# Kernel tuning notes

Measured on AMD Instinct MI355X. Metric: run time of the kernel, lower is better.

Reference implementation:

```python
import jax, jax.numpy as jnp
import numpy as np

N_HEADS = 8
DIM_HEAD = 64
SCALE = DIM_HEAD ** -0.5


def setup_inputs() -> dict:
    key = jax.random.key(0)
    ks = jax.random.split(key, 7)
    B, C, H, W = 2, 512, 64, 64
    inner = N_HEADS * DIM_HEAD  # 512
    x = jax.random.normal(ks[0], (B, C, H, W), dtype=jnp.float32)
    context = jax.random.normal(ks[1], (B, C, H, W), dtype=jnp.float32)
    # kaiming_normal fan_out for 1x1 conv: std = sqrt(2 / out_channels)
    std_qkv = (2.0 / inner) ** 0.5
    std_o = (2.0 / C) ** 0.5
    Wq = jax.random.normal(ks[2], (inner, C), dtype=jnp.float32) * std_qkv
    Wk = jax.random.normal(ks[3], (inner, C), dtype=jnp.float32) * std_qkv
    Wv = jax.random.normal(ks[4], (inner, C), dtype=jnp.float32) * std_qkv
    Wo = jax.random.normal(ks[5], (C, inner), dtype=jnp.float32) * std_o
    return {
        'x': x, 'context': context,
        'Wq': Wq, 'bq': jnp.zeros((inner,), jnp.float32),
        'Wk': Wk, 'bk': jnp.zeros((inner,), jnp.float32),
        'Wv': Wv, 'bv': jnp.zeros((inner,), jnp.float32),
        'Wo': Wo, 'bo': jnp.zeros((C,), jnp.float32),
    }


def _attention(x, context, Wq, bq, Wk, bk, Wv, bv, Wo, bo):
    b, c, h, w = x.shape
    s = h * w
    # 1x1 conv == per-pixel channel matmul. Flatten spatial: [b, s, c]
    xf = x.reshape(b, c, s).transpose(0, 2, 1)
    cf = context.reshape(b, c, s).transpose(0, 2, 1)
    q = jnp.einsum('bsc,ec->bse', xf, Wq) + bq  # [b, s, inner]
    k = jnp.einsum('bsc,ec->bse', cf, Wk) + bk
    v = jnp.einsum('bsc,ec->bse', cf, Wv) + bv
    # split heads: [b, n, s, d]
    def split(t):
        return t.reshape(b, s, N_HEADS, DIM_HEAD).transpose(0, 2, 1, 3)
    q, k, v = split(q), split(k), split(v)
    sim = jnp.einsum('bnid,bnjd->bnij', q, k) * SCALE  # [b, n, s, s]
    attn = jax.nn.softmax(sim, axis=-1)
    out = jnp.einsum('bnij,bnjd->bnid', attn, v)  # [b, n, s, d]
    # merge heads back to channels: 'b n s d -> b (n d) s'
    out = out.transpose(0, 2, 1, 3).reshape(b, s, N_HEADS * DIM_HEAD)
    out = jnp.einsum('bse,ce->bsc', out, Wo) + bo  # output proj (1x1 conv)
    return out.transpose(0, 2, 1).reshape(b, c, h, w)


def reference(x, context, Wq, bq, Wk, bk, Wv, bv, Wo, bo):
    return _attention(x, context, Wq, bq, Wk, bk, Wv, bv, Wo, bo)
```

## Files before the change

### kernel.cpp

```cpp
#include <hip/hip_runtime.h>
#include <cstdint>


typedef __bf16 bf16x8 __attribute__((ext_vector_type(8)));
typedef __bf16 bf16x4 __attribute__((ext_vector_type(4)));
typedef float f32x4 __attribute__((ext_vector_type(4)));
typedef unsigned short u16x8 __attribute__((ext_vector_type(8)));
typedef unsigned short u16x4 __attribute__((ext_vector_type(4)));

#define AS1 __attribute__((address_space(1)))
#define AS3 __attribute__((address_space(3)))

__device__ __forceinline__ void async16(const void* g, void* l) {
  __builtin_amdgcn_global_load_lds((const AS1 void*)g, (AS3 void*)l, 16, 0, 0);
}

__device__ __forceinline__ uint16_t f2bf(float f) {
  union { float f; uint32_t u; } a;
  a.f = f;
  uint32_t r = a.u + 0x7fffu + ((a.u >> 16) & 1u);
  return (uint16_t)(r >> 16);
}

__device__ __forceinline__ float bf2f(uint16_t u) {
  union { uint32_t u; float f; } a;
  a.u = (uint32_t)u << 16;
  return a.f;
}

__global__ __launch_bounds__(256) void cvt_w(
    const float* __restrict__ W0, const float* __restrict__ W1,
    const float* __restrict__ W2, const float* __restrict__ W3,
    uint16_t* __restrict__ O0, uint16_t* __restrict__ O1,
    uint16_t* __restrict__ O2, uint16_t* __restrict__ O3) {
  const float* W[4] = {W0, W1, W2, W3};
  uint16_t* O[4] = {O0, O1, O2, O3};
  const int w = blockIdx.y;
  const int i = (blockIdx.x * 256 + threadIdx.x) * 4;
  float4 v = *(const float4*)&W[w][i];
  u16x4 o = {f2bf(v.x), f2bf(v.y), f2bf(v.z), f2bf(v.w)};
  *(u16x4*)&O[w][i] = o;
}

__global__ __launch_bounds__(256) void transpose_cs(
    const float* __restrict__ x, const float* __restrict__ ctx,
    uint16_t* __restrict__ xT, uint16_t* __restrict__ cT) {
  const int zz = blockIdx.z;
  const float* src = (zz < 2 ? x : ctx) + (size_t)(zz & 1) * 512 * 4096;
  uint16_t* dst = (zz < 2 ? xT : cT) + (size_t)(zz & 1) * 4096 * 512;
  const int s0 = blockIdx.x * 64, c0 = blockIdx.y * 64;
  __shared__ uint16_t tile[64][80];
  const int t = threadIdx.x;
  for (int p = 0; p < 2; ++p) {
    int u = p * 256 + t;
    int r = u >> 3, cg = (u & 7) * 8;
    const float* sp = &src[(size_t)(c0 + r) * 4096 + s0 + cg];
    float4 v0 = *(const float4*)sp;
    float4 v1 = *(const float4*)(sp + 4);
    u16x8 o = {f2bf(v0.x), f2bf(v0.y), f2bf(v0.z), f2bf(v0.w),
               f2bf(v1.x), f2bf(v1.y), f2bf(v1.z), f2bf(v1.w)};
    *(u16x8*)&tile[r][cg] = o;
  }
  __syncthreads();
  for (int p = 0; p < 2; ++p) {
    int u = p * 256 + t;
    int sr = u >> 3, cg = (u & 7) * 8;
    u16x8 v;
    for (int j = 0; j < 8; ++j) v[j] = tile[cg + j][sr];
    *(u16x8*)&dst[(size_t)(s0 + sr) * 512 + c0 + cg] = v;
  }
}

struct QkvArgs {
  const uint16_t* A[3]; long long sA[3];
  const uint16_t* B[3]; long long sB[3];
  uint16_t* C[3];       long long sC[3];
  const float* bias[3];
  float os[3];
  long long ldC[3]; int lx[3]; int brow[3];
};

__global__ __launch_bounds__(256) void gemm_qkv(QkvArgs ga) {
  constexpr int K = 512;
  __shared__ uint16_t At[128 * 32];
  __shared__ uint16_t Bt[128 * 32];
  const int t = threadIdx.x, lane = t & 63, wave = t >> 6;
  const int lr = lane & 15, lq = lane >> 4;
  const int wm = (wave >> 1) * 64, wn = (wave & 1) * 64;
  const int sel = blockIdx.z >> 1, bat = blockIdx.z & 1;
  const int lx = ga.lx[sel], brow = ga.brow[sel];
  const long long ldC = ga.ldC[sel];
  const float os = ga.os[sel];
  const int n0 = (blockIdx.x & ((1 << lx) - 1)) * 128;
  const int m0 = (blockIdx.x >> lx) * 128;
  const uint16_t* A = ga.A[sel] + (size_t)bat * ga.sA[sel];
  const uint16_t* B = ga.B[sel] + (size_t)bat * ga.sB[sel];
  const float* bias = ga.bias[sel];
  f32x4 acc[4][4] = {};
  for (int k0 = 0; k0 < K; k0 += 32) {
    __syncthreads();
    for (int p = 0; p < 2; ++p) {
      int u = p * 256 + t;
      int r = u >> 2, c = (u & 3) * 8;
      async16(&A[(size_t)(m0 + r) * K + k0 + c], &At[p * 2048 + wave * 512]);
      async16(&B[(size_t)(n0 + r) * K + k0 + c], &Bt[p * 2048 + wave * 512]);
    }
    __builtin_amdgcn_s_waitcnt(0);
    __syncthreads();
    bf16x8 af[4], bfr[4];
    for (int i = 0; i < 4; ++i)
      af[i] = *(const bf16x8*)&At[(wm + i * 16 + lr) * 32 + lq * 8];
    for (int j = 0; j < 4; ++j)
      bfr[j] = *(const bf16x8*)&Bt[(wn + j * 16 + lr) * 32 + lq * 8];
    for (int i = 0; i < 4; ++i)
      for (int j = 0; j < 4; ++j)
        acc[i][j] = __builtin_amdgcn_mfma_f32_16x16x32_bf16(af[i], bfr[j], acc[i][j], 0, 0, 0);
  }
  uint16_t* C = ga.C[sel] + (size_t)bat * ga.sC[sel];
  for (int i = 0; i < 4; ++i)
    for (int j = 0; j < 4; ++j) {
      int row = m0 + wm + i * 16 + lq * 4;
      int col = n0 + wn + j * 16 + lr;
      float bc = brow ? 0.f : bias[col];
      u16x4 o;
      for (int r = 0; r < 4; ++r) {
        float val = (acc[i][j][r] + (brow ? bias[row + r] : bc)) * os;
        o[r] = f2bf(val);
      }
      *(u16x4*)&C[(size_t)col * ldC + row] = o;
    }
}

__global__ __launch_bounds__(256) void gemm_out(
    const uint16_t* __restrict__ Ob, long long sA,
    const uint16_t* __restrict__ Wo, float* __restrict__ Y, long long sC,
    const float* __restrict__ bias) {
  constexpr int K = 512;
  __shared__ uint16_t At[128 * 32];
  __shared__ uint16_t Bt[64 * 32];
  const int t = threadIdx.x, lane = t & 63, wave = t >> 6;
  const int lr = lane & 15, lq = lane >> 4;
  const int wm = (wave & 1) * 64, wn = (wave >> 1) * 32;
  const int m0 = blockIdx.y * 128, n0 = blockIdx.x * 64;
  const uint16_t* A = Ob + (size_t)blockIdx.z * sA;
  f32x4 acc[4][2] = {};
  for (int k0 = 0; k0 < K; k0 += 32) {
    __syncthreads();
    for (int p = 0; p < 2; ++p) {
      int u = p * 256 + t;
      int r = u >> 2, c = (u & 3) * 8;
      async16(&A[(size_t)(m0 + r) * K + k0 + c], &At[p * 2048 + wave * 512]);
    }
    {
      int r = t >> 2, c = (t & 3) * 8;
      async16(&Wo[(size_t)(n0 + r) * K + k0 + c], &Bt[wave * 512]);
    }
    __builtin_amdgcn_s_waitcnt(0);
    __syncthreads();
    bf16x8 af[4], bfr[2];
    for (int i = 0; i < 4; ++i)
      af[i] = *(const bf16x8*)&At[(wm + i * 16 + lr) * 32 + lq * 8];
    for (int j = 0; j < 2; ++j)
      bfr[j] = *(const bf16x8*)&Bt[(wn + j * 16 + lr) * 32 + lq * 8];
    for (int i = 0; i < 4; ++i)
      for (int j = 0; j < 2; ++j)
        acc[i][j] = __builtin_amdgcn_mfma_f32_16x16x32_bf16(af[i], bfr[j], acc[i][j], 0, 0, 0);
  }
  float* Cf = Y + (size_t)blockIdx.z * sC;
  for (int i = 0; i < 4; ++i)
    for (int j = 0; j < 2; ++j) {
      int row = m0 + wm + i * 16 + lq * 4;
      int col = n0 + wn + j * 16 + lr;
      float bb = bias[col];
      float4 o = {acc[i][j][0] + bb, acc[i][j][1] + bb,
                  acc[i][j][2] + bb, acc[i][j][3] + bb};
      *(float4*)&Cf[(size_t)col * 4096 + row] = o;
    }
}

__global__ __launch_bounds__(512, 4) void attn128(
    const uint16_t* __restrict__ Q, const uint16_t* __restrict__ K,
    const uint16_t* __restrict__ Vt, uint16_t* __restrict__ Ap,
    float* __restrict__ Lp) {
  constexpr int S = 4096, E = 512;
  const int b = blockIdx.z & 1, jh = blockIdx.z >> 1;
  const int h = blockIdx.y;
  const int i0 = blockIdx.x * 256;
  const int t = threadIdx.x, lane = t & 63, wave = t >> 6;
  const int lr = lane & 15, lq = lane >> 4;
  const size_t qkB = (size_t)b * S * E;
  const size_t vB = (size_t)b * E * S;
  __shared__ uint16_t Kl[2][64 * 64];
  __shared__ uint16_t Vl[2][64 * 64];

  const int qbase = i0 + wave * 32;
  bf16x8 qf[2][2];
  for (int g = 0; g < 2; ++g) {
    const size_t qo = qkB + (size_t)(qbase + g * 16 + lr) * E + h * 64 + lq * 8;
    qf[g][0] = *(const bf16x8*)&Q[qo];
    qf[g][1] = *(const bf16x8*)&Q[qo + 32];
  }
  f32x4 lsum[2] = {};
  f32x4 accOT[2][4] = {};
  const f32x4 fz = {0.f, 0.f, 0.f, 0.f};
  const int swz = (lr & 7);
  const int srr = t >> 3, ssc = ((t & 7) ^ (srr & 7)) * 8;

  const int jbeg = jh * (S / 2), jend = jbeg + S / 2;
  async16(&K[qkB + (size_t)(jbeg + srr) * E + h * 64 + ssc], &Kl[0][wave * 512]);
  async16(&Vt[vB + (size_t)(h * 64 + srr) * S + jbeg + ssc], &Vl[0][wave * 512]);
  __builtin_amdgcn_s_waitcnt(0);
  __syncthreads();

  int cur = 0;
  for (int j0 = jbeg; j0 < jend; j0 += 64) {
    if (j0 + 64 < jend) {
      async16(&K[qkB + (size_t)(j0 + 64 + srr) * E + h * 64 + ssc], &Kl[cur ^ 1][wave * 512]);
      async16(&Vt[vB + (size_t)(h * 64 + srr) * S + j0 + 64 + ssc], &Vl[cur ^ 1][wave * 512]);
    }
    const uint16_t* Kc = Kl[cur];
    const uint16_t* Vc = Vl[cur];
    f32x4 svt[2][4];
#pragma unroll
    for (int jn = 0; jn < 4; ++jn) {
      const int row = jn * 16 + lr;
      const int c0 = (lq ^ swz) * 8;
      bf16x8 ka0 = *(const bf16x8*)&Kc[row * 64 + c0];
      bf16x8 ka1 = *(const bf16x8*)&Kc[row * 64 + (c0 ^ 32)];
#pragma unroll
      for (int g = 0; g < 2; ++g) {
        f32x4 z = __builtin_amdgcn_mfma_f32_16x16x32_bf16(ka0, qf[g][0], fz, 0, 0, 0);
        z = __builtin_amdgcn_mfma_f32_16x16x32_bf16(ka1, qf[g][1], z, 0, 0, 0);
        svt[g][jn] = z;
      }
    }
    bf16x8 pa[2][2];
#pragma unroll
    for (int g = 0; g < 2; ++g) {
      uint32_t pk[4][2];
#pragma unroll
      for (int jn = 0; jn < 4; ++jn) {
        f32x4 p;
#pragma unroll
        for (int r = 0; r < 4; ++r) p[r] = __builtin_amdgcn_exp2f(svt[g][jn][r]);
        lsum[g] += p;
        asm("v_cvt_pk_bf16_f32 %0, %1, %2" : "=v"(pk[jn][0]) : "v"(p[0]), "v"(p[1]));
        asm("v_cvt_pk_bf16_f32 %0, %1, %2" : "=v"(pk[jn][1]) : "v"(p[2]), "v"(p[3]));
      }
#pragma unroll
      for (int half = 0; half < 2; ++half) {
        union { uint32_t w[4]; bf16x8 v; } f;
#pragma unroll
        for (int p_ = 0; p_ < 2; ++p_) {
          uint32_t a = pk[2 * half][p_];
          uint32_t c = pk[2 * half + 1][p_];
          asm("v_permlane32_swap_b32 %0, %1" : "+v"(a), "+v"(c));
          asm("v_permlane16_swap_b32 %0, %1" : "+v"(a), "+v"(c));
          f.w[p_] = a;
          f.w[2 + p_] = c;
        }
        pa[g][half] = f.v;
      }
    }
#pragma unroll
    for (int dn = 0; dn < 4; ++dn) {
      const int row = dn * 16 + lr;
      const int c0 = (lq ^ swz) * 8;
      bf16x8 v0 = *(const bf16x8*)&Vc[row * 64 + c0];
      bf16x8 v1 = *(const bf16x8*)&Vc[row * 64 + (c0 ^ 32)];
#pragma unroll
      for (int g = 0; g < 2; ++g) {
        accOT[g][dn] = __builtin_amdgcn_mfma_f32_16x16x32_bf16(v0, pa[g][0], accOT[g][dn], 0, 0, 0);
        accOT[g][dn] = __builtin_amdgcn_mfma_f32_16x16x32_bf16(v1, pa[g][1], accOT[g][dn], 0, 0, 0);
      }
    }
    __builtin_amdgcn_s_waitcnt(0);
    __syncthreads();
    cur ^= 1;
  }
  uint16_t* Aph = Ap + (size_t)jh * 2 * S * E;
  float* Lph = Lp + ((size_t)(jh * 2 + b) * 8 + h) * S;
  for (int g = 0; g < 2; ++g) {
    float lt = (lsum[g][0] + lsum[g][1]) + (lsum[g][2] + lsum[g][3]);
    lt += __shfl_xor(lt, 16);
    lt += __shfl_xor(lt, 32);
    if (lane < 16) Lph[qbase + g * 16 + lr] = lt;
    const size_t row = qbase + g * 16 + lr;
    for (int dn = 0; dn < 4; ++dn) {
      u16x4 o;
      for (int r = 0; r < 4; ++r) o[r] = f2bf(accOT[g][dn][r]);
      *(u16x4*)&Aph[qkB + row * E + h * 64 + dn * 16 + lq * 4] = o;
    }
  }
}

__global__ __launch_bounds__(256) void attn_combine(
    const uint16_t* __restrict__ Ap, const float* __restrict__ Lp,
    uint16_t* __restrict__ Ob) {
  constexpr int S = 4096, E = 512;
  const size_t HALF = (size_t)2 * S * E;
  const size_t idx = ((size_t)blockIdx.x * 256 + threadIdx.x) * 4;
  const int b = (int)(idx / ((size_t)S * E));
  const size_t rem = idx % ((size_t)S * E);
  const int s = (int)(rem / E), e = (int)(rem % E);
  const int h = e >> 6;
  const float l0 = Lp[((size_t)(0 * 2 + b) * 8 + h) * S + s];
  const float l1 = Lp[((size_t)(1 * 2 + b) * 8 + h) * S + s];
  const float inv = 1.f / (l0 + l1);
  u16x4 a0 = *(const u16x4*)&Ap[idx];
  u16x4 a1 = *(const u16x4*)&Ap[HALF + idx];
  u16x4 o;
  for (int r = 0; r < 4; ++r) o[r] = f2bf((bf2f(a0[r]) + bf2f(a1[r])) * inv);
  *(u16x4*)&Ob[idx] = o;
}

extern "C" void kernel_launch(void* const* d_in, const int* in_sizes, int n_in,
                              void* d_out, int out_size, void* d_ws, size_t ws_size,
                              hipStream_t stream) {
  const float* x   = (const float*)d_in[0];
  const float* ctx = (const float*)d_in[1];
  const float* Wq  = (const float*)d_in[2];
  const float* bq  = (const float*)d_in[3];
  const float* Wk  = (const float*)d_in[4];
  const float* bk  = (const float*)d_in[5];
  const float* Wv  = (const float*)d_in[6];
  const float* bv  = (const float*)d_in[7];
  const float* Wo  = (const float*)d_in[8];
  const float* bo  = (const float*)d_in[9];
  float* out = (float*)d_out;

  const size_t SZ = (size_t)2 * 4096 * 512;
  uint16_t* xT = (uint16_t*)d_ws;
  uint16_t* cT = xT + SZ;
  uint16_t* Qb = cT + SZ;
  uint16_t* Kb = Qb + SZ;
  uint16_t* Vb = Kb + SZ;
  uint16_t* Ob = Vb + SZ;
  uint16_t* Wqb = Ob + SZ;
  uint16_t* Wkb = Wqb + 512 * 512;
  uint16_t* Wvb = Wkb + 512 * 512;
  uint16_t* Wob = Wvb + 512 * 512;
  uint16_t* Ap  = Wob + 512 * 512;
  float*    Lp  = (float*)(Ap + 2 * SZ);
  const long long sIn = 4096LL * 512LL;
  const float slh = 0.125f * 1.44269504088896f;

  cvt_w<<<dim3(256, 4), 256, 0, stream>>>(Wq, Wk, Wv, Wo, Wqb, Wkb, Wvb, Wob);
  transpose_cs<<<dim3(64, 8, 4), 256, 0, stream>>>(x, ctx, xT, cT);
  QkvArgs qkv = {
      {Wqb, Wkb, cT}, {0, 0, sIn},
      {xT, cT, Wvb}, {sIn, sIn, 0},
      {Qb, Kb, Vb}, {sIn, sIn, sIn},
      {bq, bk, bv},
      {slh, 1.f, 1.f},
      {512, 512, 4096},
      {5, 5, 2},
      {1, 1, 0}};
  gemm_qkv<<<dim3(128, 1, 6), 256, 0, stream>>>(qkv);
  attn128<<<dim3(16, 8, 4), 512, 0, stream>>>(Qb, Kb, Vb, Ap, Lp);
  attn_combine<<<dim3(4096), 256, 0, stream>>>(Ap, Lp, Ob);
  gemm_out<<<dim3(8, 32, 2), 256, 0, stream>>>(Ob, sIn, Wob, out, sIn, bo);
}
```

Baseline: 224.8 us.

## Split attention keys into four chunks and compute row sums with MFMA

The attention kernel now splits the key range into quarters instead of halves, doubling the grid to 1024 blocks, and raises the launch-bounds occupancy hint. Row sums of the exponentials are accumulated with an MFMA against a vector of bf16 ones, replacing per-element VALU adds and the final cross-lane shuffles. The combine kernel now merges four bf16 partial outputs and four partial sums, and the freed input-transpose buffer is reused for two of the partials. The aim is to fill more CUs during attention. In exchange, the combine step moves more partial-output traffic, and the tighter register budget implied by the new launch bound may cause spills.

```diff
diff --git a/kernel.cpp b/kernel.cpp
--- a/kernel.cpp
+++ b/kernel.cpp
@@ -178,12 +178,13 @@
     }
 }
 
-__global__ __launch_bounds__(512, 4) void attn128(
+__global__ __launch_bounds__(512, 8) void attn128(
     const uint16_t* __restrict__ Q, const uint16_t* __restrict__ K,
-    const uint16_t* __restrict__ Vt, uint16_t* __restrict__ Ap,
-    float* __restrict__ Lp) {
+    const uint16_t* __restrict__ Vt, uint16_t* __restrict__ ApA,
+    uint16_t* __restrict__ ApB, float* __restrict__ Lp) {
   constexpr int S = 4096, E = 512;
-  const int b = blockIdx.z & 1, jh = blockIdx.z >> 1;
+  constexpr size_t QSZ = (size_t)2 * S * E;
+  const int b = blockIdx.z & 1, jq = blockIdx.z >> 1;
   const int h = blockIdx.y;
   const int i0 = blockIdx.x * 256;
   const int t = threadIdx.x, lane = t & 63, wave = t >> 6;
@@ -200,13 +201,16 @@
     qf[g][0] = *(const bf16x8*)&Q[qo];
     qf[g][1] = *(const bf16x8*)&Q[qo + 32];
   }
-  f32x4 lsum[2] = {};
+  union { u16x8 u; bf16x8 v; } onesu;
+  for (int i = 0; i < 8; ++i) onesu.u[i] = 0x3F80;
+  const bf16x8 ones = onesu.v;
+  f32x4 lacc[2] = {};
   f32x4 accOT[2][4] = {};
   const f32x4 fz = {0.f, 0.f, 0.f, 0.f};
   const int swz = (lr & 7);
   const int srr = t >> 3, ssc = ((t & 7) ^ (srr & 7)) * 8;
 
-  const int jbeg = jh * (S / 2), jend = jbeg + S / 2;
+  const int jbeg = jq * (S / 4), jend = jbeg + S / 4;
   async16(&K[qkB + (size_t)(jbeg + srr) * E + h * 64 + ssc], &Kl[0][wave * 512]);
   async16(&Vt[vB + (size_t)(h * 64 + srr) * S + jbeg + ssc], &Vl[0][wave * 512]);
   __builtin_amdgcn_s_waitcnt(0);
@@ -243,7 +247,6 @@
         f32x4 p;
 #pragma unroll
         for (int r = 0; r < 4; ++r) p[r] = __builtin_amdgcn_exp2f(svt[g][jn][r]);
-        lsum[g] += p;
         asm("v_cvt_pk_bf16_f32 %0, %1, %2" : "=v"(pk[jn][0]) : "v"(p[0]), "v"(p[1]));
         asm("v_cvt_pk_bf16_f32 %0, %1, %2" : "=v"(pk[jn][1]) : "v"(p[2]), "v"(p[3]));
       }
@@ -261,6 +264,8 @@
         }
         pa[g][half] = f.v;
       }
+      lacc[g] = __builtin_amdgcn_mfma_f32_16x16x32_bf16(ones, pa[g][0], lacc[g], 0, 0, 0);
+      lacc[g] = __builtin_amdgcn_mfma_f32_16x16x32_bf16(ones, pa[g][1], lacc[g], 0, 0, 0);
     }
 #pragma unroll
     for (int dn = 0; dn < 4; ++dn) {
@@ -278,13 +283,10 @@
     __syncthreads();
     cur ^= 1;
   }
-  uint16_t* Aph = Ap + (size_t)jh * 2 * S * E;
-  float* Lph = Lp + ((size_t)(jh * 2 + b) * 8 + h) * S;
+  uint16_t* Aph = (jq < 2 ? ApA : ApB) + (size_t)(jq & 1) * QSZ;
+  float* Lph = Lp + ((size_t)(jq * 2 + b) * 8 + h) * S;
   for (int g = 0; g < 2; ++g) {
-    float lt = (lsum[g][0] + lsum[g][1]) + (lsum[g][2] + lsum[g][3]);
-    lt += __shfl_xor(lt, 16);
-    lt += __shfl_xor(lt, 32);
-    if (lane < 16) Lph[qbase + g * 16 + lr] = lt;
+    if (lane < 16) Lph[qbase + g * 16 + lr] = lacc[g][0];
     const size_t row = qbase + g * 16 + lr;
     for (int dn = 0; dn < 4; ++dn) {
       u16x4 o;
@@ -295,22 +297,26 @@
 }
 
 __global__ __launch_bounds__(256) void attn_combine(
-    const uint16_t* __restrict__ Ap, const float* __restrict__ Lp,
-    uint16_t* __restrict__ Ob) {
+    const uint16_t* __restrict__ ApA, const uint16_t* __restrict__ ApB,
+    const float* __restrict__ Lp, uint16_t* __restrict__ Ob) {
   constexpr int S = 4096, E = 512;
-  const size_t HALF = (size_t)2 * S * E;
+  const size_t QSZ = (size_t)2 * S * E;
   const size_t idx = ((size_t)blockIdx.x * 256 + threadIdx.x) * 4;
   const int b = (int)(idx / ((size_t)S * E));
   const size_t rem = idx % ((size_t)S * E);
   const int s = (int)(rem / E), e = (int)(rem % E);
   const int h = e >> 6;
-  const float l0 = Lp[((size_t)(0 * 2 + b) * 8 + h) * S + s];
-  const float l1 = Lp[((size_t)(1 * 2 + b) * 8 + h) * S + s];
-  const float inv = 1.f / (l0 + l1);
-  u16x4 a0 = *(const u16x4*)&Ap[idx];
-  u16x4 a1 = *(const u16x4*)&Ap[HALF + idx];
+  float l = 0.f;
+  for (int q = 0; q < 4; ++q)
+    l += Lp[((size_t)(q * 2 + b) * 8 + h) * S + s];
+  const float inv = 1.f / l;
+  u16x4 a0 = *(const u16x4*)&ApA[idx];
+  u16x4 a1 = *(const u16x4*)&ApA[QSZ + idx];
+  u16x4 a2 = *(const u16x4*)&ApB[idx];
+  u16x4 a3 = *(const u16x4*)&ApB[QSZ + idx];
   u16x4 o;
-  for (int r = 0; r < 4; ++r) o[r] = f2bf((bf2f(a0[r]) + bf2f(a1[r])) * inv);
+  for (int r = 0; r < 4; ++r)
+    o[r] = f2bf((bf2f(a0[r]) + bf2f(a1[r]) + bf2f(a2[r]) + bf2f(a3[r])) * inv);
   *(u16x4*)&Ob[idx] = o;
 }
 
@@ -340,8 +346,9 @@
   uint16_t* Wkb = Wqb + 512 * 512;
   uint16_t* Wvb = Wkb + 512 * 512;
   uint16_t* Wob = Wvb + 512 * 512;
-  uint16_t* Ap  = Wob + 512 * 512;
-  float*    Lp  = (float*)(Ap + 2 * SZ);
+  uint16_t* ApB = Wob + 512 * 512;
+  float*    Lp  = (float*)(ApB + 2 * SZ);
+  uint16_t* ApA = xT;
   const long long sIn = 4096LL * 512LL;
   const float slh = 0.125f * 1.44269504088896f;
 
@@ -357,7 +364,7 @@
       {5, 5, 2},
       {1, 1, 0}};
   gemm_qkv<<<dim3(128, 1, 6), 256, 0, stream>>>(qkv);
-  attn128<<<dim3(16, 8, 4), 512, 0, stream>>>(Qb, Kb, Vb, Ap, Lp);
-  attn_combine<<<dim3(4096), 256, 0, stream>>>(Ap, Lp, Ob);
+  attn128<<<dim3(16, 8, 8), 512, 0, stream>>>(Qb, Kb, Vb, ApA, ApB, Lp);
+  attn_combine<<<dim3(4096), 256, 0, stream>>>(ApA, ApB, Lp, Ob);
   gemm_out<<<dim3(8, 32, 2), 256, 0, stream>>>(Ob, sIn, Wob, out, sIn, bo);
 }
```

Result: slower. 733.1 us (+226.0%).
